# Performance work log

Measured on AMD Instinct MI355X. Metric: run time of the kernel, lower is better.

## Reference

```python
import jax, jax.numpy as jnp
import numpy as np

N, E, D = 50000, 600000, 128
EPS_BN = 1e-5
EPS_ETA = 1e-6


def _lin_params(key, din, dout):
    kw, kb = jax.random.split(key)
    s = 1.0 / np.sqrt(din)
    w = jax.random.uniform(kw, (dout, din), jnp.float32, -s, s)
    b = jax.random.uniform(kb, (dout,), jnp.float32, -s, s)
    return w, b


def setup_inputs() -> dict:
    key = jax.random.key(0)
    ks = jax.random.split(key, 12)
    h = jax.random.normal(ks[0], (N, D), jnp.float32)
    e = jax.random.normal(ks[1], (E, D), jnp.float32)
    p = jax.random.normal(ks[2], (N, D), jnp.float32)
    src = jax.random.randint(ks[3], (E,), 0, N, jnp.int32)
    dst = jax.random.randint(ks[4], (E,), 0, N, jnp.int32)
    A1w, A1b = _lin_params(ks[5], D, D)
    A2w, A2b = _lin_params(ks[6], 2 * D, D)
    B1w, B1b = _lin_params(ks[7], D, D)
    B2w, B2b = _lin_params(ks[8], D, D)
    B3w, B3b = _lin_params(ks[9], D, D)
    C1w, C1b = _lin_params(ks[10], D, D)
    C2w, C2b = _lin_params(ks[11], D, D)
    bn_h_g = jnp.ones((D,), jnp.float32); bn_h_b = jnp.zeros((D,), jnp.float32)
    bn_e_g = jnp.ones((D,), jnp.float32); bn_e_b = jnp.zeros((D,), jnp.float32)
    return dict(h=h, e=e, p=p, src=src, dst=dst,
                A1w=A1w, A1b=A1b, A2w=A2w, A2b=A2b,
                B1w=B1w, B1b=B1b, B2w=B2w, B2b=B2b, B3w=B3w, B3b=B3b,
                C1w=C1w, C1b=C1b, C2w=C2w, C2b=C2b,
                bn_h_g=bn_h_g, bn_h_b=bn_h_b, bn_e_g=bn_e_g, bn_e_b=bn_e_b)


def _lin(x, w, b):
    return x @ w.T + b


def _bn(x, g, b):
    m = x.mean(0)
    v = x.var(0)  # biased, as in torch BatchNorm1d training normalization
    return g * (x - m) * jax.lax.rsqrt(v + EPS_BN) + b


def reference(h, e, p, src, dst,
              A1w, A1b, A2w, A2b, B1w, B1b, B2w, B2b, B3w, B3b,
              C1w, C1b, C2w, C2b, bn_h_g, bn_h_b, bn_e_g, bn_e_b):
    n = h.shape[0]
    # edge gate: sigma(B1 h_src + B2 h_dst + B3 e)
    hat_eta = _lin(h, B1w, B1b)[src] + _lin(h, B2w, B2b)[dst] + _lin(e, B3w, B3b)  # [E,D]
    sigma = jax.nn.sigmoid(hat_eta)
    sum_sigma = jax.ops.segment_sum(sigma, dst, num_segments=n)  # [N,D]
    eta = sigma / (sum_sigma[dst] + EPS_ETA)  # [E,D]
    # v_ij = A2([h_src; p_src])
    v = _lin(jnp.concatenate([h[src], p[src]], -1), A2w, A2b)
    h_new = _lin(h, A1w, A1b) + jax.ops.segment_sum(eta * v, dst, num_segments=n)
    # p update
    c2p = _lin(p, C2w, C2b)[src]
    p_new = _lin(p, C1w, C1b) + jax.ops.segment_sum(eta * c2p, dst, num_segments=n)
    e_new = hat_eta
    h_out = jax.nn.relu(_bn(h_new, bn_h_g, bn_h_b))
    e_out = jax.nn.relu(_bn(e_new, bn_e_g, bn_e_b))
    p_out = jnp.tanh(p_new)
    # residual (input_dim == output_dim)
    h_out = h + h_out
    p_out = p + p_out
    e_out = e + e_out
    return h_out, e_out, p_out
```

## Files before the change

kernel.cpp:

```cpp
#include <hip/hip_runtime.h>
#include <math.h>

#define D 128
#define BM 64
#define BN 128
#define BK 32

__global__ __launch_bounds__(256) void gemm_node(
    const float* __restrict__ in0, const float* __restrict__ in1,
    const float* __restrict__ w, const float* __restrict__ bias,
    float* __restrict__ out, int R, int din)
{
    __shared__ float sIn[BM][BK + 1];
    __shared__ alignas(16) float sW[BK][BN + 4];
    const int tid = threadIdx.x;
    const int r0 = blockIdx.x * BM;
    const int cg = tid & 31;
    const int rg = tid >> 5;

    float acc[8][4] = {};

    for (int k0 = 0; k0 < din; k0 += BK) {
#pragma unroll
        for (int l = 0; l < 8; ++l) {
            int lin = l * 256 + tid;
            int r = lin >> 5;
            int kk = lin & 31;
            int gr = r0 + r;
            float v = 0.f;
            if (gr < R) {
                int k = k0 + kk;
                v = (k < 128) ? in0[(size_t)gr * 128 + k]
                              : in1[(size_t)gr * 128 + (k - 128)];
            }
            sIn[r][kk] = v;
        }
#pragma unroll
        for (int l = 0; l < 16; ++l) {
            int lin = l * 256 + tid;
            int c = lin >> 5;
            int kk = lin & 31;
            sW[kk][c] = w[(size_t)c * din + k0 + kk];
        }
        __syncthreads();
#pragma unroll
        for (int kk = 0; kk < BK; ++kk) {
            const float4 bv = *reinterpret_cast<const float4*>(&sW[kk][cg * 4]);
            float a[8];
#pragma unroll
            for (int i = 0; i < 8; ++i) a[i] = sIn[rg * 8 + i][kk];
#pragma unroll
            for (int i = 0; i < 8; ++i) {
                acc[i][0] += a[i] * bv.x;
                acc[i][1] += a[i] * bv.y;
                acc[i][2] += a[i] * bv.z;
                acc[i][3] += a[i] * bv.w;
            }
        }
        __syncthreads();
    }

    const float4 bvb = *reinterpret_cast<const float4*>(&bias[cg * 4]);
#pragma unroll
    for (int i = 0; i < 8; ++i) {
        int gr = r0 + rg * 8 + i;
        if (gr < R) {
            float4 o;
            o.x = acc[i][0] + bvb.x;
            o.y = acc[i][1] + bvb.y;
            o.z = acc[i][2] + bvb.z;
            o.w = acc[i][3] + bvb.w;
            *reinterpret_cast<float4*>(&out[(size_t)gr * 128 + cg * 4]) = o;
        }
    }
}

__global__ __launch_bounds__(256) void gemm_edge(
    const float* __restrict__ e, const float* __restrict__ w,
    const float* __restrict__ bias,
    const float* __restrict__ B1h, const float* __restrict__ B2h,
    const int* __restrict__ src, const int* __restrict__ dst,
    float* __restrict__ hat_eta, int E)
{
    __shared__ float sIn[BM][BK + 1];
    __shared__ alignas(16) float sW[BK][BN + 4];
    __shared__ int sSrc[BM];
    __shared__ int sDst[BM];
    const int tid = threadIdx.x;
    const int r0 = blockIdx.x * BM;
    const int cg = tid & 31;
    const int rg = tid >> 5;

    if (tid < BM) {
        int gr = r0 + tid;
        sSrc[tid] = (gr < E) ? src[gr] : 0;
        sDst[tid] = (gr < E) ? dst[gr] : 0;
    }

    float acc[8][4] = {};

    for (int k0 = 0; k0 < 128; k0 += BK) {
#pragma unroll
        for (int l = 0; l < 8; ++l) {
            int lin = l * 256 + tid;
            int r = lin >> 5;
            int kk = lin & 31;
            int gr = r0 + r;
            sIn[r][kk] = (gr < E) ? e[(size_t)gr * 128 + k0 + kk] : 0.f;
        }
#pragma unroll
        for (int l = 0; l < 16; ++l) {
            int lin = l * 256 + tid;
            int c = lin >> 5;
            int kk = lin & 31;
            sW[kk][c] = w[(size_t)c * 128 + k0 + kk];
        }
        __syncthreads();
#pragma unroll
        for (int kk = 0; kk < BK; ++kk) {
            const float4 bv = *reinterpret_cast<const float4*>(&sW[kk][cg * 4]);
            float a[8];
#pragma unroll
            for (int i = 0; i < 8; ++i) a[i] = sIn[rg * 8 + i][kk];
#pragma unroll
            for (int i = 0; i < 8; ++i) {
                acc[i][0] += a[i] * bv.x;
                acc[i][1] += a[i] * bv.y;
                acc[i][2] += a[i] * bv.z;
                acc[i][3] += a[i] * bv.w;
            }
        }
        __syncthreads();
    }

    const float4 bvb = *reinterpret_cast<const float4*>(&bias[cg * 4]);
#pragma unroll
    for (int i = 0; i < 8; ++i) {
        int r = rg * 8 + i;
        int gr = r0 + r;
        if (gr < E) {
            const int sn = sSrc[r];
            const int dn = sDst[r];
            const float4 b1 = *reinterpret_cast<const float4*>(&B1h[(size_t)sn * 128 + cg * 4]);
            const float4 b2 = *reinterpret_cast<const float4*>(&B2h[(size_t)dn * 128 + cg * 4]);
            float4 o;
            o.x = acc[i][0] + bvb.x + b1.x + b2.x;
            o.y = acc[i][1] + bvb.y + b1.y + b2.y;
            o.z = acc[i][2] + bvb.z + b1.z + b2.z;
            o.w = acc[i][3] + bvb.w + b1.w + b2.w;
            *reinterpret_cast<float4*>(&hat_eta[(size_t)gr * 128 + cg * 4]) = o;
        }
    }
}

__global__ __launch_bounds__(256) void csr_count(
    const int* __restrict__ dst, int* __restrict__ cnt, int E_)
{
    int e = blockIdx.x * 256 + threadIdx.x;
    if (e < E_) atomicAdd(&cnt[dst[e]], 1);
}

__global__ __launch_bounds__(1024) void csr_scan(
    int* __restrict__ cursor, int* __restrict__ ioff, int n)
{
    __shared__ int tmp[1024];
    __shared__ int carry;
    const int tid = threadIdx.x;
    if (tid == 0) carry = 0;
    __syncthreads();
    for (int base = 0; base < n; base += 1024) {
        int i = base + tid;
        int v = (i < n) ? cursor[i] : 0;
        int x = v;
        tmp[tid] = x;
        __syncthreads();
        for (int s = 1; s < 1024; s <<= 1) {
            int y = (tid >= s) ? tmp[tid - s] : 0;
            __syncthreads();
            x += y;
            tmp[tid] = x;
            __syncthreads();
        }
        int excl = x - v + carry;
        if (i < n) { ioff[i] = excl; cursor[i] = excl; }
        int total = tmp[1023];
        __syncthreads();
        if (tid == 0) carry += total;
        __syncthreads();
    }
    if (tid == 0) ioff[n] = carry;
}

__global__ __launch_bounds__(256) void csr_scatter(
    const int* __restrict__ dst, int* __restrict__ cursor,
    int* __restrict__ eids, int E_)
{
    int e = blockIdx.x * 256 + threadIdx.x;
    if (e < E_) {
        int p = atomicAdd(&cursor[dst[e]], 1);
        eids[p] = e;
    }
}

__global__ __launch_bounds__(256) void node_aggregate(
    const float* __restrict__ hat_eta,
    const int* __restrict__ ioff, const int* __restrict__ eids,
    const int* __restrict__ src,
    const float* __restrict__ A2hp, const float* __restrict__ C2p,
    float* __restrict__ h_new, const float* __restrict__ C1p,
    const float* __restrict__ p, float* __restrict__ out_p,
    float* __restrict__ h_stats, float* __restrict__ e_stats, int Nn)
{
    const int tid = threadIdx.x;
    const int d = tid & 127;
    const int half = tid >> 7;
    float e1 = 0.f, e2 = 0.f, hs1 = 0.f, hs2 = 0.f;
    for (int n = blockIdx.x * 2 + half; n < Nn; n += gridDim.x * 2) {
        const int beg = ioff[n];
        const int end = ioff[n + 1];
        float ss = 0.f, hacc = 0.f, pacc = 0.f;
        for (int t = beg; t < end; ++t) {
            const int ed = eids[t];
            const int sn = src[ed];
            const float he = hat_eta[(size_t)ed * 128 + d];
            e1 += he;
            e2 += he * he;
            const float sg = 1.f / (1.f + expf(-he));
            ss += sg;
            hacc += sg * A2hp[(size_t)sn * 128 + d];
            pacc += sg * C2p[(size_t)sn * 128 + d];
        }
        const float inv = 1.f / (ss + 1e-6f);
        const size_t idx = (size_t)n * 128 + d;
        const float hv = h_new[idx] + hacc * inv;
        h_new[idx] = hv;
        hs1 += hv;
        hs2 += hv * hv;
        out_p[idx] = p[idx] + tanhf(C1p[idx] + pacc * inv);
    }
    __shared__ float red[256];
    red[tid] = e1; __syncthreads();
    if (tid < 128) atomicAdd(&e_stats[d], red[tid] + red[tid + 128]);
    __syncthreads(); red[tid] = e2; __syncthreads();
    if (tid < 128) atomicAdd(&e_stats[128 + d], red[tid] + red[tid + 128]);
    __syncthreads(); red[tid] = hs1; __syncthreads();
    if (tid < 128) atomicAdd(&h_stats[d], red[tid] + red[tid + 128]);
    __syncthreads(); red[tid] = hs2; __syncthreads();
    if (tid < 128) atomicAdd(&h_stats[128 + d], red[tid] + red[tid + 128]);
}

__global__ __launch_bounds__(256) void finalize_bn_relu_res(
    const float* __restrict__ resid, const float* __restrict__ xnew,
    const float* __restrict__ stats, const float* __restrict__ g,
    const float* __restrict__ bb, float* __restrict__ out,
    size_t total, float invR)
{
    size_t idx = (size_t)blockIdx.x * 256 + threadIdx.x;
    if (idx >= total) return;
    int d = (int)(idx & 127);
    float m = stats[d] * invR;
    float var = stats[128 + d] * invR - m * m;
    if (var < 0.f) var = 0.f;
    float x = xnew[idx];
    float y = g[d] * (x - m) * rsqrtf(var + 1e-5f) + bb[d];
    y = y > 0.f ? y : 0.f;
    out[idx] = resid[idx] + y;
}

extern "C" void kernel_launch(void* const* d_in, const int* in_sizes, int n_in,
                              void* d_out, int out_size, void* d_ws, size_t ws_size,
                              hipStream_t stream)
{
    const float* h   = (const float*)d_in[0];
    const float* e   = (const float*)d_in[1];
    const float* p   = (const float*)d_in[2];
    const int* src   = (const int*)d_in[3];
    const int* dst   = (const int*)d_in[4];
    const float* A1w = (const float*)d_in[5];
    const float* A1b = (const float*)d_in[6];
    const float* A2w = (const float*)d_in[7];
    const float* A2b = (const float*)d_in[8];
    const float* B1w = (const float*)d_in[9];
    const float* B1b = (const float*)d_in[10];
    const float* B2w = (const float*)d_in[11];
    const float* B2b = (const float*)d_in[12];
    const float* B3w = (const float*)d_in[13];
    const float* B3b = (const float*)d_in[14];
    const float* C1w = (const float*)d_in[15];
    const float* C1b = (const float*)d_in[16];
    const float* C2w = (const float*)d_in[17];
    const float* C2b = (const float*)d_in[18];
    const float* bn_h_g = (const float*)d_in[19];
    const float* bn_h_b = (const float*)d_in[20];
    const float* bn_e_g = (const float*)d_in[21];
    const float* bn_e_b = (const float*)d_in[22];

    const int N = in_sizes[0] / D;
    const int E = in_sizes[3];
    const size_t ND = (size_t)N * D;
    const size_t ED = (size_t)E * D;

    float* out_h = (float*)d_out;
    float* out_e = out_h + ND;
    float* out_p = out_e + ED;

    float* ws = (float*)d_ws;
    float* B1h    = ws;
    float* B2h    = B1h + ND;
    float* A2hp   = B2h + ND;
    float* C2p    = A2hp + ND;
    float* h_new  = C2p + ND;
    float* C1p    = h_new + ND;
    float* stats  = C1p + ND;
    int*   ioff   = (int*)(stats + 512);
    int*   cursor = ioff + (N + 1);
    int*   eids   = cursor + N;

    hipMemsetAsync(stats, 0,
                   512 * sizeof(float) + (size_t)(2 * N + 1) * sizeof(int),
                   stream);

    const int gN = (N + BM - 1) / BM;
    const int gE = (E + BM - 1) / BM;
    const int gEt = (E + 255) / 256;

    csr_count<<<gEt, 256, 0, stream>>>(dst, cursor, E);

    gemm_node<<<gN, 256, 0, stream>>>(h, nullptr, A1w, A1b, h_new, N, 128);
    gemm_node<<<gN, 256, 0, stream>>>(h, nullptr, B1w, B1b, B1h, N, 128);
    gemm_node<<<gN, 256, 0, stream>>>(h, nullptr, B2w, B2b, B2h, N, 128);
    gemm_node<<<gN, 256, 0, stream>>>(p, nullptr, C1w, C1b, C1p, N, 128);
    gemm_node<<<gN, 256, 0, stream>>>(p, nullptr, C2w, C2b, C2p, N, 128);
    gemm_node<<<gN, 256, 0, stream>>>(h, p, A2w, A2b, A2hp, N, 256);

    csr_scan<<<1, 1024, 0, stream>>>(cursor, ioff, N);
    csr_scatter<<<gEt, 256, 0, stream>>>(dst, cursor, eids, E);

    gemm_edge<<<gE, 256, 0, stream>>>(e, B3w, B3b, B1h, B2h, src, dst,
                                      out_e, E);

    node_aggregate<<<2048, 256, 0, stream>>>(out_e, ioff, eids, src,
                                             A2hp, C2p, h_new, C1p, p, out_p,
                                             stats, stats + 256, N);

    {
        int blocks = (int)((ND + 255) / 256);
        finalize_bn_relu_res<<<blocks, 256, 0, stream>>>(
            h, h_new, stats, bn_h_g, bn_h_b, out_h, ND, 1.f / (float)N);
    }
    {
        int blocks = (int)((ED + 255) / 256);
        finalize_bn_relu_res<<<blocks, 256, 0, stream>>>(
            e, out_e, stats + 256, bn_e_g, bn_e_b, out_e, ED, 1.f / (float)E);
    }
}
```

Measured before the change: 2.028 ms.

## Enlarge GEMM tiles to 256x128 with 16x8 register blocking and swizzled LDS

Both node and edge GEMM kernels now use 256-row tiles with each thread computing a 16x8 output block. Inputs and weights are loaded with float4 global reads and stored transposed into shared memory with an XOR swizzle, so the inner loop can read float4 vectors without bank conflicts. The aim is more FMA per shared-memory load and better global coalescing. In exchange, 128 accumulators per thread raise register pressure, which lowers occupancy, and larger tiles mean fewer blocks for the smaller node GEMMs.

New measurement: 1.773 ms. 12.6% less time.

```diff
diff --git a/kernel.cpp b/kernel.cpp
--- a/kernel.cpp
+++ b/kernel.cpp
@@ -2,7 +2,7 @@
 #include <math.h>
 
 #define D 128
-#define BM 64
+#define BM 256
 #define BN 128
 #define BK 32
 
@@ -11,66 +11,89 @@
     const float* __restrict__ w, const float* __restrict__ bias,
     float* __restrict__ out, int R, int din)
 {
-    __shared__ float sIn[BM][BK + 1];
-    __shared__ alignas(16) float sW[BK][BN + 4];
+    __shared__ float sIn[BK][BM + 4];
+    __shared__ float sW[BK][BN + 4];
     const int tid = threadIdx.x;
     const int r0 = blockIdx.x * BM;
-    const int cg = tid & 31;
-    const int rg = tid >> 5;
-
-    float acc[8][4] = {};
+    const int cg = tid & 15;
+    const int rg = tid >> 4;
+    const int s_kk4 = tid & 7;
+    const int s_r   = tid >> 3;
+
+    float acc[16][8] = {};
 
     for (int k0 = 0; k0 < din; k0 += BK) {
 #pragma unroll
         for (int l = 0; l < 8; ++l) {
-            int lin = l * 256 + tid;
-            int r = lin >> 5;
-            int kk = lin & 31;
+            int r = s_r + l * 32;
             int gr = r0 + r;
-            float v = 0.f;
+            float4 v = {0.f, 0.f, 0.f, 0.f};
             if (gr < R) {
-                int k = k0 + kk;
-                v = (k < 128) ? in0[(size_t)gr * 128 + k]
-                              : in1[(size_t)gr * 128 + (k - 128)];
+                int k = k0 + s_kk4 * 4;
+                const float* base = (k < 128)
+                    ? &in0[(size_t)gr * 128 + k]
+                    : &in1[(size_t)gr * 128 + (k - 128)];
+                v = *reinterpret_cast<const float4*>(base);
             }
-            sIn[r][kk] = v;
-        }
-#pragma unroll
-        for (int l = 0; l < 16; ++l) {
-            int lin = l * 256 + tid;
-            int c = lin >> 5;
-            int kk = lin & 31;
-            sW[kk][c] = w[(size_t)c * din + k0 + kk];
-        }
-        __syncthreads();
-#pragma unroll
+            int col = r ^ (s_kk4 << 2);
+            sIn[s_kk4 * 4 + 0][col] = v.x;
+            sIn[s_kk4 * 4 + 1][col] = v.y;
+            sIn[s_kk4 * 4 + 2][col] = v.z;
+            sIn[s_kk4 * 4 + 3][col] = v.w;
+        }
+#pragma unroll
+        for (int l = 0; l < 4; ++l) {
+            int c = s_r + l * 32;
+            float4 v = *reinterpret_cast<const float4*>(
+                &w[(size_t)c * din + k0 + s_kk4 * 4]);
+            int col = c ^ (s_kk4 << 2);
+            sW[s_kk4 * 4 + 0][col] = v.x;
+            sW[s_kk4 * 4 + 1][col] = v.y;
+            sW[s_kk4 * 4 + 2][col] = v.z;
+            sW[s_kk4 * 4 + 3][col] = v.w;
+        }
+        __syncthreads();
+#pragma unroll 4
         for (int kk = 0; kk < BK; ++kk) {
-            const float4 bv = *reinterpret_cast<const float4*>(&sW[kk][cg * 4]);
-            float a[8];
-#pragma unroll
-            for (int i = 0; i < 8; ++i) a[i] = sIn[rg * 8 + i][kk];
-#pragma unroll
-            for (int i = 0; i < 8; ++i) {
-                acc[i][0] += a[i] * bv.x;
-                acc[i][1] += a[i] * bv.y;
-                acc[i][2] += a[i] * bv.z;
-                acc[i][3] += a[i] * bv.w;
+            const int X = (kk >> 2) << 2;
+            float a[16], b[8];
+#pragma unroll
+            for (int q = 0; q < 4; ++q) {
+                float4 t = *reinterpret_cast<const float4*>(
+                    &sIn[kk][(rg * 16 + q * 4) ^ X]);
+                a[q * 4 + 0] = t.x; a[q * 4 + 1] = t.y;
+                a[q * 4 + 2] = t.z; a[q * 4 + 3] = t.w;
             }
-        }
-        __syncthreads();
-    }
-
-    const float4 bvb = *reinterpret_cast<const float4*>(&bias[cg * 4]);
-#pragma unroll
-    for (int i = 0; i < 8; ++i) {
-        int gr = r0 + rg * 8 + i;
+#pragma unroll
+            for (int q = 0; q < 2; ++q) {
+                float4 t = *reinterpret_cast<const float4*>(
+                    &sW[kk][(cg * 8 + q * 4) ^ X]);
+                b[q * 4 + 0] = t.x; b[q * 4 + 1] = t.y;
+                b[q * 4 + 2] = t.z; b[q * 4 + 3] = t.w;
+            }
+#pragma unroll
+            for (int i = 0; i < 16; ++i)
+#pragma unroll
+                for (int j = 0; j < 8; ++j)
+                    acc[i][j] += a[i] * b[j];
+        }
+        __syncthreads();
+    }
+
+    const float4 bv0 = *reinterpret_cast<const float4*>(&bias[cg * 8]);
+    const float4 bv1 = *reinterpret_cast<const float4*>(&bias[cg * 8 + 4]);
+#pragma unroll
+    for (int i = 0; i < 16; ++i) {
+        int gr = r0 + rg * 16 + i;
         if (gr < R) {
-            float4 o;
-            o.x = acc[i][0] + bvb.x;
-            o.y = acc[i][1] + bvb.y;
-            o.z = acc[i][2] + bvb.z;
-            o.w = acc[i][3] + bvb.w;
-            *reinterpret_cast<float4*>(&out[(size_t)gr * 128 + cg * 4]) = o;
+            float4 o0, o1;
+            o0.x = acc[i][0] + bv0.x; o0.y = acc[i][1] + bv0.y;
+            o0.z = acc[i][2] + bv0.z; o0.w = acc[i][3] + bv0.w;
+            o1.x = acc[i][4] + bv1.x; o1.y = acc[i][5] + bv1.y;
+            o1.z = acc[i][6] + bv1.z; o1.w = acc[i][7] + bv1.w;
+            float* op = &out[(size_t)gr * 128 + cg * 8];
+            *reinterpret_cast<float4*>(op) = o0;
+            *reinterpret_cast<float4*>(op + 4) = o1;
         }
     }
 }
@@ -82,73 +105,106 @@
     const int* __restrict__ src, const int* __restrict__ dst,
     float* __restrict__ hat_eta, int E)
 {
-    __shared__ float sIn[BM][BK + 1];
-    __shared__ alignas(16) float sW[BK][BN + 4];
+    __shared__ float sIn[BK][BM + 4];
+    __shared__ float sW[BK][BN + 4];
     __shared__ int sSrc[BM];
     __shared__ int sDst[BM];
     const int tid = threadIdx.x;
     const int r0 = blockIdx.x * BM;
-    const int cg = tid & 31;
-    const int rg = tid >> 5;
-
-    if (tid < BM) {
+    const int cg = tid & 15;
+    const int rg = tid >> 4;
+    const int s_kk4 = tid & 7;
+    const int s_r   = tid >> 3;
+
+    {
         int gr = r0 + tid;
         sSrc[tid] = (gr < E) ? src[gr] : 0;
         sDst[tid] = (gr < E) ? dst[gr] : 0;
     }
 
-    float acc[8][4] = {};
+    float acc[16][8] = {};
 
     for (int k0 = 0; k0 < 128; k0 += BK) {
 #pragma unroll
         for (int l = 0; l < 8; ++l) {
-            int lin = l * 256 + tid;
-            int r = lin >> 5;
-            int kk = lin & 31;
+            int r = s_r + l * 32;
             int gr = r0 + r;
-            sIn[r][kk] = (gr < E) ? e[(size_t)gr * 128 + k0 + kk] : 0.f;
-        }
-#pragma unroll
-        for (int l = 0; l < 16; ++l) {
-            int lin = l * 256 + tid;
-            int c = lin >> 5;
-            int kk = lin & 31;
-            sW[kk][c] = w[(size_t)c * 128 + k0 + kk];
-        }
-        __syncthreads();
-#pragma unroll
+            float4 v = {0.f, 0.f, 0.f, 0.f};
+            if (gr < E)
+                v = *reinterpret_cast<const float4*>(
+                    &e[(size_t)gr * 128 + k0 + s_kk4 * 4]);
+            int col = r ^ (s_kk4 << 2);
+            sIn[s_kk4 * 4 + 0][col] = v.x;
+            sIn[s_kk4 * 4 + 1][col] = v.y;
+            sIn[s_kk4 * 4 + 2][col] = v.z;
+            sIn[s_kk4 * 4 + 3][col] = v.w;
+        }
+#pragma unroll
+        for (int l = 0; l < 4; ++l) {
+            int c = s_r + l * 32;
+            float4 v = *reinterpret_cast<const float4*>(
+                &w[(size_t)c * 128 + k0 + s_kk4 * 4]);
+            int col = c ^ (s_kk4 << 2);
+            sW[s_kk4 * 4 + 0][col] = v.x;
+            sW[s_kk4 * 4 + 1][col] = v.y;
+            sW[s_kk4 * 4 + 2][col] = v.z;
+            sW[s_kk4 * 4 + 3][col] = v.w;
+        }
+        __syncthreads();
+#pragma unroll 4
         for (int kk = 0; kk < BK; ++kk) {
-            const float4 bv = *reinterpret_cast<const float4*>(&sW[kk][cg * 4]);
-            float a[8];
-#pragma unroll
-            for (int i = 0; i < 8; ++i) a[i] = sIn[rg * 8 + i][kk];
-#pragma unroll
-            for (int i = 0; i < 8; ++i) {
-                acc[i][0] += a[i] * bv.x;
-                acc[i][1] += a[i] * bv.y;
-                acc[i][2] += a[i] * bv.z;
-                acc[i][3] += a[i] * bv.w;
+            const int X = (kk >> 2) << 2;
+            float a[16], b[8];
+#pragma unroll
+            for (int q = 0; q < 4; ++q) {
+                float4 t = *reinterpret_cast<const float4*>(
+                    &sIn[kk][(rg * 16 + q * 4) ^ X]);
+                a[q * 4 + 0] = t.x; a[q * 4 + 1] = t.y;
+                a[q * 4 + 2] = t.z; a[q * 4 + 3] = t.w;
             }
-        }
-        __syncthreads();
-    }
-
-    const float4 bvb = *reinterpret_cast<const float4*>(&bias[cg * 4]);
-#pragma unroll
-    for (int i = 0; i < 8; ++i) {
-        int r = rg * 8 + i;
+#pragma unroll
+            for (int q = 0; q < 2; ++q) {
+                float4 t = *reinterpret_cast<const float4*>(
+                    &sW[kk][(cg * 8 + q * 4) ^ X]);
+                b[q * 4 + 0] = t.x; b[q * 4 + 1] = t.y;
+                b[q * 4 + 2] = t.z; b[q * 4 + 3] = t.w;
+            }
+#pragma unroll
+            for (int i = 0; i < 16; ++i)
+#pragma unroll
+                for (int j = 0; j < 8; ++j)
+                    acc[i][j] += a[i] * b[j];
+        }
+        __syncthreads();
+    }
+
+    const float4 bv0 = *reinterpret_cast<const float4*>(&bias[cg * 8]);
+    const float4 bv1 = *reinterpret_cast<const float4*>(&bias[cg * 8 + 4]);
+#pragma unroll
+    for (int i = 0; i < 16; ++i) {
+        int r = rg * 16 + i;
         int gr = r0 + r;
         if (gr < E) {
             const int sn = sSrc[r];
             const int dn = sDst[r];
-            const float4 b1 = *reinterpret_cast<const float4*>(&B1h[(size_t)sn * 128 + cg * 4]);
-            const float4 b2 = *reinterpret_cast<const float4*>(&B2h[(size_t)dn * 128 + cg * 4]);
-            float4 o;
-            o.x = acc[i][0] + bvb.x + b1.x + b2.x;
-            o.y = acc[i][1] + bvb.y + b1.y + b2.y;
-            o.z = acc[i][2] + bvb.z + b1.z + b2.z;
-            o.w = acc[i][3] + bvb.w + b1.w + b2.w;
-            *reinterpret_cast<float4*>(&hat_eta[(size_t)gr * 128 + cg * 4]) = o;
+            const float* p1 = &B1h[(size_t)sn * 128 + cg * 8];
+            const float* p2 = &B2h[(size_t)dn * 128 + cg * 8];
+            const float4 a1 = *reinterpret_cast<const float4*>(p1);
+            const float4 a2 = *reinterpret_cast<const float4*>(p1 + 4);
+            const float4 c1 = *reinterpret_cast<const float4*>(p2);
+            const float4 c2 = *reinterpret_cast<const float4*>(p2 + 4);
+            float4 o0, o1;
+            o0.x = acc[i][0] + bv0.x + a1.x + c1.x;
+            o0.y = acc[i][1] + bv0.y + a1.y + c1.y;
+            o0.z = acc[i][2] + bv0.z + a1.z + c1.z;
+            o0.w = acc[i][3] + bv0.w + a1.w + c1.w;
+            o1.x = acc[i][4] + bv1.x + a2.x + c2.x;
+            o1.y = acc[i][5] + bv1.y + a2.y + c2.y;
+            o1.z = acc[i][6] + bv1.z + a2.z + c2.z;
+            o1.w = acc[i][7] + bv1.w + a2.w + c2.w;
+            float* op = &hat_eta[(size_t)gr * 128 + cg * 8];
+            *reinterpret_cast<float4*>(op) = o0;
+            *reinterpret_cast<float4*>(op + 4) = o1;
         }
     }
 }
```
